# Performance work log

Hardware: AMD Instinct MI355X
Metric: run time of the kernel (lower is better)

## Reference

```python
import jax, jax.numpy as jnp
import numpy as np

D_MODEL, D_K, D_V = 1024, 64, 64
B, S = 4, 4096

def setup_inputs() -> dict:
    key = jax.random.key(0)
    ks = jax.random.split(key, 9)
    s_in = 1.0 / np.sqrt(D_MODEL)
    return {
        "Q": jax.random.normal(ks[0], (B, S, D_MODEL), jnp.float32),
        "K": jax.random.normal(ks[1], (B, S, D_MODEL), jnp.float32),
        "V": jax.random.normal(ks[2], (B, S, D_MODEL), jnp.float32),
        "Wq": jax.random.uniform(ks[3], (D_MODEL, D_K), jnp.float32, -s_in, s_in),
        "bq": jax.random.uniform(ks[4], (D_K,), jnp.float32, -s_in, s_in),
        "Wk": jax.random.uniform(ks[5], (D_MODEL, D_K), jnp.float32, -s_in, s_in),
        "bk": jax.random.uniform(ks[6], (D_K,), jnp.float32, -s_in, s_in),
        "Wv": jax.random.uniform(ks[7], (D_MODEL, D_V), jnp.float32, -s_in, s_in),
        "bv": jax.random.uniform(ks[8], (D_V,), jnp.float32, -s_in, s_in),
    }

def reference(Q, K, V, Wq, bq, Wk, bk, Wv, bv):
    # Linear projections: [B,S,d_model] -> [B,S,d_k/d_v]
    q = jnp.einsum("bsm,mk->bsk", Q, Wq) + bq
    k = jnp.einsum("btm,mk->btk", K, Wk) + bk
    v = jnp.einsum("btm,mv->btv", V, Wv) + bv
    # Scaled dot-product attention, softmax over key axis (dim=2)
    scores = jnp.einsum("bsk,btk->bst", q, k) / jnp.sqrt(jnp.float32(D_K))
    attn = jax.nn.softmax(scores, axis=2)  # [B,S,S]
    return jnp.einsum("bst,btv->bsv", attn, v)
```

## Files before the change

### kernel.cpp

```cpp
#include <hip/hip_runtime.h>

typedef __bf16 bf16;
typedef __attribute__((ext_vector_type(4))) __bf16 bf16x4;
typedef __attribute__((ext_vector_type(8))) __bf16 bf16x8;
typedef __attribute__((ext_vector_type(4))) float f32x4;
typedef __attribute__((ext_vector_type(16))) float f32x16;

#define MFMA16(a, b, c) __builtin_amdgcn_mfma_f32_16x16x32_bf16((a), (b), (c), 0, 0, 0)
#define MFMA32(a, b, c) __builtin_amdgcn_mfma_f32_32x32x16_bf16((a), (b), (c), 0, 0, 0)

__device__ __forceinline__ bf16 tobf(float f) {
    unsigned u = __float_as_uint(f);
    u += 0x7fffu + ((u >> 16) & 1u);
    unsigned short h = (unsigned short)(u >> 16);
    bf16 r;
    __builtin_memcpy(&r, &h, 2);
    return r;
}

__device__ __forceinline__ void stage16(const void* g, void* l) {
    __builtin_amdgcn_global_load_lds(
        (const __attribute__((address_space(1))) unsigned int*)g,
        (__attribute__((address_space(3))) unsigned int*)l, 16, 0, 0);
}

__global__ void wconv_kernel(const float* __restrict__ Wq, const float* __restrict__ Wk,
                             const float* __restrict__ Wv, bf16* __restrict__ Wt) {
    int j = blockIdx.y;
    const float* W = (j == 0) ? Wq : ((j == 1) ? Wk : Wv);
    int idx = blockIdx.x * 256 + threadIdx.x;
    int m = idx >> 6, n = idx & 63;
    Wt[(size_t)j * 65536 + (size_t)n * 1024 + m] = tobf(W[idx]);
}

__launch_bounds__(256, 3)
__global__ void proj_kernel(const float* __restrict__ Q, const float* __restrict__ K,
                            const float* __restrict__ V, const bf16* __restrict__ Wt,
                            const float* __restrict__ bq, const float* __restrict__ bk,
                            const float* __restrict__ bv,
                            bf16* __restrict__ q_ws, bf16* __restrict__ k_ws,
                            bf16* __restrict__ vT_ws) {
    const int j = blockIdx.y;
    const float* In   = (j == 0) ? Q : ((j == 1) ? K : V);
    const float* bias = (j == 0) ? bq : ((j == 1) ? bk : bv);
    const bf16* W = Wt + (size_t)j * 65536;

    __shared__ float As[2][64][64];

    const int tid = threadIdx.x;
    const int wave = tid >> 6, lane = tid & 63;
    const int quad = lane >> 4, l16 = lane & 15;
    const int rbase = blockIdx.x * 64;

    const char* asrc[4];
    char* adst0[4];
    char* adst1[4];
#pragma unroll
    for (int i = 0; i < 4; i++) {
        int u = i * 256 + tid;
        int row = u >> 4;
        int rg = ((u & 15) * 16) ^ ((row & 7) << 4);
        asrc[i] = (const char*)(In + (size_t)(rbase + row) * 1024) + rg;
        adst0[i] = (char*)&As[0][0][0] + u * 16;
        adst1[i] = (char*)&As[1][0][0] + u * 16;
    }

#pragma unroll
    for (int i = 0; i < 4; i++) stage16(asrc[i], adst0[i]);
    __syncthreads();

    f32x4 acc[4];
#pragma unroll
    for (int nt = 0; nt < 4; nt++) acc[nt] = {0.f, 0.f, 0.f, 0.f};

    const int row = wave * 16 + l16;
    const char* arow = (const char*)&As[0][row][0];
    const int sw = (l16 & 7) << 4;
    const bf16* wrow = W + quad * 8;

#pragma unroll 2
    for (int t = 0; t < 16; ++t) {
        const int cur = t & 1;
        if (t < 15) {
#pragma unroll
            for (int i = 0; i < 4; i++)
                stage16(asrc[i] + (t + 1) * 256, cur ? adst0[i] : adst1[i]);
        }
        bf16x8 bf[2][4];
#pragma unroll
        for (int c = 0; c < 2; c++)
#pragma unroll
            for (int nt = 0; nt < 4; nt++)
                bf[c][nt] = *(const bf16x8*)(wrow + (size_t)(nt * 16 + l16) * 1024 +
                                             t * 64 + c * 32);
        const char* ab = arow + (size_t)cur * 16384;
#pragma unroll
        for (int c = 0; c < 2; c++) {
            f32x4 a0 = *(const f32x4*)(ab + ((c * 128 + quad * 32) ^ sw));
            f32x4 a1 = *(const f32x4*)(ab + ((c * 128 + quad * 32 + 16) ^ sw));
            bf16x8 av;
            av[0] = (bf16)a0[0]; av[1] = (bf16)a0[1];
            av[2] = (bf16)a0[2]; av[3] = (bf16)a0[3];
            av[4] = (bf16)a1[0]; av[5] = (bf16)a1[1];
            av[6] = (bf16)a1[2]; av[7] = (bf16)a1[3];
#pragma unroll
            for (int nt = 0; nt < 4; nt++) acc[nt] = MFMA16(av, bf[c][nt], acc[nt]);
        }
        __syncthreads();
    }

    const float scale = (j == 0) ? 0.125f * 1.44269504088896f : 1.0f;

    if (j != 2) {
        bf16* dst = (j == 0) ? q_ws : k_ws;
#pragma unroll
        for (int nt = 0; nt < 4; nt++) {
            int n = nt * 16 + l16;
            float bb = bias[n];
#pragma unroll
            for (int r4 = 0; r4 < 4; r4++) {
                int orow = rbase + wave * 16 + quad * 4 + r4;
                dst[(size_t)orow * 64 + n] = tobf((acc[nt][r4] + bb) * scale);
            }
        }
    } else {
        bf16 (*vtile)[72] = (bf16(*)[72])As;
#pragma unroll
        for (int nt = 0; nt < 4; nt++) {
            int n = nt * 16 + l16;
            float bb = bias[n];
#pragma unroll
            for (int r4 = 0; r4 < 4; r4++) {
                vtile[n][wave * 16 + quad * 4 + r4] = tobf(acc[nt][r4] + bb);
            }
        }
        __syncthreads();
        int bi = rbase >> 12, t0 = rbase & 4095;
        int d = tid >> 2, part = (tid & 3) * 16;
        bf16x8 x0 = *(const bf16x8*)&vtile[d][part];
        bf16x8 x1 = *(const bf16x8*)&vtile[d][part + 8];
        bf16* dst = vT_ws + (size_t)(bi * 64 + d) * 4096 + t0 + part;
        *(bf16x8*)dst = x0;
        *(bf16x8*)(dst + 8) = x1;
    }
}

__launch_bounds__(256, 4)
__global__ void attn_kernel(const bf16* __restrict__ q_ws, const bf16* __restrict__ k_ws,
                            const bf16* __restrict__ vT_ws,
                            float* __restrict__ po, float* __restrict__ pl,
                            float* __restrict__ out, int keys_per_split, int direct) {
    const int b = blockIdx.z, split = blockIdx.y;
    const int tid = threadIdx.x, wave = tid >> 6, lane = tid & 63;
    const int l32 = lane & 31, h = lane >> 5;
    const int sw = l32 & 7;

    __shared__ bf16 kt[64][64];
    __shared__ bf16 vt[64][64];
    __shared__ bf16 pt[4][32][64];

    const int qrow0 = b * 4096 + blockIdx.x * 128 + wave * 32;

    bf16x8 qf[4];
    const bf16* qp = q_ws + (size_t)(qrow0 + l32) * 64 + h * 8;
#pragma unroll
    for (int c = 0; c < 4; c++) qf[c] = *(const bf16x8*)(qp + c * 16);

    f32x16 o0, o1;
    float l_lane = 0.f;
#pragma unroll
    for (int i = 0; i < 16; i++) { o0[i] = 0.f; o1[i] = 0.f; }

    const int key0 = split * keys_per_split;
    const int srow = tid >> 3;
    const int sg = tid & 7;
    const int sgk = sg ^ (srow & 7);
    const bf16* kg = k_ws + (size_t)(b * 4096 + key0 + srow) * 64 + sg * 8;
    const bf16* vg = vT_ws + (size_t)(b * 64 + srow) * 4096 + key0 + sg * 8;

    uint4 kv0 = *(const uint4*)kg;
    uint4 kv1 = *(const uint4*)(kg + 2048);
    uint4 vv0 = *(const uint4*)vg;
    uint4 vv1 = *(const uint4*)(vg + 131072);

    for (int t0 = 0; t0 < keys_per_split; t0 += 64) {
        __syncthreads();
        *(uint4*)&kt[srow][sgk * 8]      = kv0;
        *(uint4*)&kt[srow + 32][sgk * 8] = kv1;
        *(uint4*)&vt[srow][sgk * 8]      = vv0;
        *(uint4*)&vt[srow + 32][sgk * 8] = vv1;
        if (t0 + 64 < keys_per_split) {
            kv0 = *(const uint4*)(kg + (size_t)(t0 + 64) * 64);
            kv1 = *(const uint4*)(kg + (size_t)(t0 + 64) * 64 + 2048);
            vv0 = *(const uint4*)(vg + t0 + 64);
            vv1 = *(const uint4*)(vg + t0 + 64 + 131072);
        }
        __syncthreads();

#pragma unroll
        for (int kt32 = 0; kt32 < 2; kt32++) {
            f32x16 s;
#pragma unroll
            for (int i = 0; i < 16; i++) s[i] = 0.f;
#pragma unroll
            for (int c = 0; c < 4; c++) {
                bf16x8 kf = *(const bf16x8*)(&kt[kt32 * 32 + l32][((2 * c + h) ^ sw) * 8]);
                s = MFMA32(kf, qf[c], s);
            }
#pragma unroll
            for (int g = 0; g < 4; g++) {
                float p0 = __builtin_amdgcn_exp2f(s[4 * g + 0]);
                float p1 = __builtin_amdgcn_exp2f(s[4 * g + 1]);
                float p2 = __builtin_amdgcn_exp2f(s[4 * g + 2]);
                float p3 = __builtin_amdgcn_exp2f(s[4 * g + 3]);
                l_lane += (p0 + p1) + (p2 + p3);
                bf16x4 pk;
                pk[0] = (bf16)p0; pk[1] = (bf16)p1; pk[2] = (bf16)p2; pk[3] = (bf16)p3;
                int gp = (kt32 * 4 + g) ^ sw;
                *(bf16x4*)(&pt[wave][l32][gp * 8 + 4 * h]) = pk;
            }
        }

#pragma unroll
        for (int tc = 0; tc < 4; tc++) {
            int gp = ((2 * tc + h) ^ sw) * 8;
            bf16x8 pf  = *(const bf16x8*)(&pt[wave][l32][gp]);
            bf16x8 vf0 = *(const bf16x8*)(&vt[l32][gp]);
            bf16x8 vf1 = *(const bf16x8*)(&vt[32 + l32][gp]);
            o0 = MFMA32(pf, vf0, o0);
            o1 = MFMA32(pf, vf1, o1);
        }
    }

    l_lane += __shfl_xor(l_lane, 32);

    if (direct) {
        float* orow = out + (size_t)qrow0 * 64;
#pragma unroll
        for (int i = 0; i < 16; i++) {
            int R = (i & 3) + 8 * (i >> 2) + 4 * h;
            float inv = 1.0f / __shfl(l_lane, R);
            orow[(size_t)R * 64 + l32]      = o0[i] * inv;
            orow[(size_t)R * 64 + 32 + l32] = o1[i] * inv;
        }
    } else {
        size_t prow = (size_t)split * 16384 + qrow0;
        float* pob = po + prow * 64;
#pragma unroll
        for (int i = 0; i < 16; i++) {
            int R = (i & 3) + 8 * (i >> 2) + 4 * h;
            pob[(size_t)R * 64 + l32]      = o0[i];
            pob[(size_t)R * 64 + 32 + l32] = o1[i];
        }
        if (h == 0) pl[prow + l32] = l_lane;
    }
}

__launch_bounds__(256)
__global__ void combine_kernel(const float* __restrict__ po, const float* __restrict__ pl,
                               float* __restrict__ out, int nsplit) {
    int idx = blockIdx.x * 256 + threadIdx.x;
    int row = idx >> 6;
    float so = 0.f, sl = 0.f;
    for (int s = 0; s < nsplit; s++) {
        so += po[(size_t)s * 1048576 + idx];
        sl += pl[(size_t)s * 16384 + row];
    }
    out[idx] = so / sl;
}

extern "C" void kernel_launch(void* const* d_in, const int* in_sizes, int n_in,
                              void* d_out, int out_size, void* d_ws, size_t ws_size,
                              hipStream_t stream) {
    const float* Q  = (const float*)d_in[0];
    const float* K  = (const float*)d_in[1];
    const float* V  = (const float*)d_in[2];
    const float* Wq = (const float*)d_in[3];
    const float* bq = (const float*)d_in[4];
    const float* Wk = (const float*)d_in[5];
    const float* bk = (const float*)d_in[6];
    const float* Wv = (const float*)d_in[7];
    const float* bv = (const float*)d_in[8];
    float* out = (float*)d_out;

    char* ws = (char*)d_ws;
    bf16* Wt    = (bf16*)ws;
    bf16* q_ws  = (bf16*)(ws + 393216);
    bf16* k_ws  = (bf16*)(ws + 393216 + 2097152);
    bf16* vT_ws = (bf16*)(ws + 393216 + 2 * 2097152);
    const size_t base = 393216 + 3 * 2097152;

    const size_t per_split = 16384u * 4u + 1048576u * 4u;
    int nsplit = 1;
    if (ws_size >= base + 8 * per_split) nsplit = 8;
    else if (ws_size >= base + 4 * per_split) nsplit = 4;
    else if (ws_size >= base + 2 * per_split) nsplit = 2;

    float* pl = (float*)(ws + base);
    float* po = (float*)(ws + base + (size_t)nsplit * 65536);

    hipLaunchKernelGGL(wconv_kernel, dim3(256, 3), dim3(256), 0, stream, Wq, Wk, Wv, Wt);
    hipLaunchKernelGGL(proj_kernel, dim3(256, 3), dim3(256), 0, stream,
                       Q, K, V, Wt, bq, bk, bv, q_ws, k_ws, vT_ws);
    hipLaunchKernelGGL(attn_kernel, dim3(32, nsplit, 4), dim3(256), 0, stream,
                       q_ws, k_ws, vT_ws, po, pl, out, 4096 / nsplit, nsplit == 1 ? 1 : 0);
    if (nsplit > 1) {
        hipLaunchKernelGGL(combine_kernel, dim3(4096), dim3(256), 0, stream, po, pl, out, nsplit);
    }
}
```

Measured before the change: 254.4 us.

## Replace LDS-staged projection loop with direct-to-register triple-buffered global loads

Drops the LDS double buffer for the projection's fp32 input tiles. Each lane now loads its own A fragments and W fragments straight into registers with inline-asm global_load_dwordx4. A 3-slot register ring is managed with explicit vmcnt waits and sched barriers, so there are no per-iteration __syncthreads. This is meant to remove LDS round-trips and block-wide barriers in a memory-bound projection, at the cost of more VGPRs, less coalesced per-lane access, and fragile hand-managed waitcnt ordering.

```diff
diff --git a/kernel.cpp b/kernel.cpp
--- a/kernel.cpp
+++ b/kernel.cpp
@@ -16,12 +16,6 @@
     bf16 r;
     __builtin_memcpy(&r, &h, 2);
     return r;
-}
-
-__device__ __forceinline__ void stage16(const void* g, void* l) {
-    __builtin_amdgcn_global_load_lds(
-        (const __attribute__((address_space(1))) unsigned int*)g,
-        (__attribute__((address_space(3))) unsigned int*)l, 16, 0, 0);
 }
 
 __global__ void wconv_kernel(const float* __restrict__ Wq, const float* __restrict__ Wk,
@@ -45,69 +39,70 @@
     const float* bias = (j == 0) ? bq : ((j == 1) ? bk : bv);
     const bf16* W = Wt + (size_t)j * 65536;
 
-    __shared__ float As[2][64][64];
+    __shared__ bf16 vtile[64][72];
 
     const int tid = threadIdx.x;
     const int wave = tid >> 6, lane = tid & 63;
     const int quad = lane >> 4, l16 = lane & 15;
     const int rbase = blockIdx.x * 64;
-
-    const char* asrc[4];
-    char* adst0[4];
-    char* adst1[4];
-#pragma unroll
-    for (int i = 0; i < 4; i++) {
-        int u = i * 256 + tid;
-        int row = u >> 4;
-        int rg = ((u & 15) * 16) ^ ((row & 7) << 4);
-        asrc[i] = (const char*)(In + (size_t)(rbase + row) * 1024) + rg;
-        adst0[i] = (char*)&As[0][0][0] + u * 16;
-        adst1[i] = (char*)&As[1][0][0] + u * 16;
-    }
-
-#pragma unroll
-    for (int i = 0; i < 4; i++) stage16(asrc[i], adst0[i]);
-    __syncthreads();
+    const int r0 = rbase + wave * 16;
+
+    unsigned aoff = ((unsigned)(r0 + l16) * 1024u + (unsigned)quad * 8u) * 4u;
+    unsigned boff = ((unsigned)l16 * 1024u + (unsigned)quad * 8u) * 2u;
+    const bf16* Wb0 = W;
+    const bf16* Wb1 = W + 16384;
+    const bf16* Wb2 = W + 32768;
+    const bf16* Wb3 = W + 49152;
+
+    f32x4 a0[3], a1[3];
+    bf16x8 bb[3][4];
+
+#define ISSUE(sl)                                                                          \
+    do {                                                                                   \
+        asm volatile("global_load_dwordx4 %0, %1, %2 offset:0"                             \
+                     : "=v"(a0[sl]) : "v"(aoff), "s"(In));                                 \
+        asm volatile("global_load_dwordx4 %0, %1, %2 offset:16"                            \
+                     : "=v"(a1[sl]) : "v"(aoff), "s"(In));                                 \
+        asm volatile("global_load_dwordx4 %0, %1, %2 offset:0"                             \
+                     : "=v"(bb[sl][0]) : "v"(boff), "s"(Wb0));                             \
+        asm volatile("global_load_dwordx4 %0, %1, %2 offset:0"                             \
+                     : "=v"(bb[sl][1]) : "v"(boff), "s"(Wb1));                             \
+        asm volatile("global_load_dwordx4 %0, %1, %2 offset:0"                             \
+                     : "=v"(bb[sl][2]) : "v"(boff), "s"(Wb2));                             \
+        asm volatile("global_load_dwordx4 %0, %1, %2 offset:0"                             \
+                     : "=v"(bb[sl][3]) : "v"(boff), "s"(Wb3));                             \
+        aoff += 128u;                                                                      \
+        boff += 64u;                                                                       \
+    } while (0)
+
+    ISSUE(0);
+    ISSUE(1);
+    ISSUE(2);
 
     f32x4 acc[4];
 #pragma unroll
     for (int nt = 0; nt < 4; nt++) acc[nt] = {0.f, 0.f, 0.f, 0.f};
 
-    const int row = wave * 16 + l16;
-    const char* arow = (const char*)&As[0][row][0];
-    const int sw = (l16 & 7) << 4;
-    const bf16* wrow = W + quad * 8;
-
-#pragma unroll 2
-    for (int t = 0; t < 16; ++t) {
-        const int cur = t & 1;
-        if (t < 15) {
-#pragma unroll
-            for (int i = 0; i < 4; i++)
-                stage16(asrc[i] + (t + 1) * 256, cur ? adst0[i] : adst1[i]);
-        }
-        bf16x8 bf[2][4];
-#pragma unroll
-        for (int c = 0; c < 2; c++)
-#pragma unroll
-            for (int nt = 0; nt < 4; nt++)
-                bf[c][nt] = *(const bf16x8*)(wrow + (size_t)(nt * 16 + l16) * 1024 +
-                                             t * 64 + c * 32);
-        const char* ab = arow + (size_t)cur * 16384;
-#pragma unroll
-        for (int c = 0; c < 2; c++) {
-            f32x4 a0 = *(const f32x4*)(ab + ((c * 128 + quad * 32) ^ sw));
-            f32x4 a1 = *(const f32x4*)(ab + ((c * 128 + quad * 32 + 16) ^ sw));
-            bf16x8 av;
-            av[0] = (bf16)a0[0]; av[1] = (bf16)a0[1];
-            av[2] = (bf16)a0[2]; av[3] = (bf16)a0[3];
-            av[4] = (bf16)a1[0]; av[5] = (bf16)a1[1];
-            av[6] = (bf16)a1[2]; av[7] = (bf16)a1[3];
-#pragma unroll
-            for (int nt = 0; nt < 4; nt++) acc[nt] = MFMA16(av, bf[c][nt], acc[nt]);
-        }
-        __syncthreads();
-    }
+#pragma unroll
+    for (int s = 0; s < 32; ++s) {
+        const int sl = s % 3;
+        if (s < 30)       asm volatile("s_waitcnt vmcnt(12)" ::: "memory");
+        else if (s == 30) asm volatile("s_waitcnt vmcnt(6)" ::: "memory");
+        else              asm volatile("s_waitcnt vmcnt(0)" ::: "memory");
+        __builtin_amdgcn_sched_barrier(0);
+
+        bf16x8 av;
+        av[0] = (bf16)a0[sl][0]; av[1] = (bf16)a0[sl][1];
+        av[2] = (bf16)a0[sl][2]; av[3] = (bf16)a0[sl][3];
+        av[4] = (bf16)a1[sl][0]; av[5] = (bf16)a1[sl][1];
+        av[6] = (bf16)a1[sl][2]; av[7] = (bf16)a1[sl][3];
+#pragma unroll
+        for (int nt = 0; nt < 4; nt++) acc[nt] = MFMA16(av, bb[sl][nt], acc[nt]);
+
+        __builtin_amdgcn_sched_barrier(0);
+        if (s <= 28) ISSUE(sl);
+    }
+#undef ISSUE
 
     const float scale = (j == 0) ? 0.125f * 1.44269504088896f : 1.0f;
 
@@ -116,22 +111,21 @@
 #pragma unroll
         for (int nt = 0; nt < 4; nt++) {
             int n = nt * 16 + l16;
-            float bb = bias[n];
+            float bb_ = bias[n];
 #pragma unroll
             for (int r4 = 0; r4 < 4; r4++) {
                 int orow = rbase + wave * 16 + quad * 4 + r4;
-                dst[(size_t)orow * 64 + n] = tobf((acc[nt][r4] + bb) * scale);
+                dst[(size_t)orow * 64 + n] = tobf((acc[nt][r4] + bb_) * scale);
             }
         }
     } else {
-        bf16 (*vtile)[72] = (bf16(*)[72])As;
 #pragma unroll
         for (int nt = 0; nt < 4; nt++) {
             int n = nt * 16 + l16;
-            float bb = bias[n];
+            float bb_ = bias[n];
 #pragma unroll
             for (int r4 = 0; r4 < 4; r4++) {
-                vtile[n][wave * 16 + quad * 4 + r4] = tobf(acc[nt][r4] + bb);
+                vtile[n][wave * 16 + quad * 4 + r4] = tobf(acc[nt][r4] + bb_);
             }
         }
         __syncthreads();
```

Measured after the change: 262.4 us. 1.03x slower.

## Restructure projection kernel to stage full 16-row panels with one wave per output column block

Applied to the files above, without the earlier changes.

The projection kernel now gives each block 16 input rows, where it previously took 64. It loads the full 16x1024 fp32 panel into LDS in a single pass and drops the double-buffered K-loop. Each wave computes one 16-column output tile over the full reduction, so the grid grows to 1024x3 blocks. The aim is more blocks in flight to hide HBM latency on a bandwidth-bound fp32 read, at the cost of 64KB LDS per block (lower occupancy), no load/compute overlap within a block, and smaller transposed V stores.

```diff
diff --git a/kernel.cpp b/kernel.cpp
--- a/kernel.cpp
+++ b/kernel.cpp
@@ -33,7 +33,7 @@
     Wt[(size_t)j * 65536 + (size_t)n * 1024 + m] = tobf(W[idx]);
 }
 
-__launch_bounds__(256, 3)
+__launch_bounds__(256, 2)
 __global__ void proj_kernel(const float* __restrict__ Q, const float* __restrict__ K,
                             const float* __restrict__ V, const bf16* __restrict__ Wt,
                             const float* __restrict__ bq, const float* __restrict__ bk,
@@ -45,103 +45,68 @@
     const float* bias = (j == 0) ? bq : ((j == 1) ? bk : bv);
     const bf16* W = Wt + (size_t)j * 65536;
 
-    __shared__ float As[2][64][64];
+    __shared__ float As[16][1024];
 
     const int tid = threadIdx.x;
     const int wave = tid >> 6, lane = tid & 63;
     const int quad = lane >> 4, l16 = lane & 15;
-    const int rbase = blockIdx.x * 64;
-
-    const char* asrc[4];
-    char* adst0[4];
-    char* adst1[4];
-#pragma unroll
-    for (int i = 0; i < 4; i++) {
-        int u = i * 256 + tid;
-        int row = u >> 4;
-        int rg = ((u & 15) * 16) ^ ((row & 7) << 4);
-        asrc[i] = (const char*)(In + (size_t)(rbase + row) * 1024) + rg;
-        adst0[i] = (char*)&As[0][0][0] + u * 16;
-        adst1[i] = (char*)&As[1][0][0] + u * 16;
-    }
-
-#pragma unroll
-    for (int i = 0; i < 4; i++) stage16(asrc[i], adst0[i]);
+    const int r0 = blockIdx.x * 16;
+
+    {
+        const char* pansrc = (const char*)(In + (size_t)r0 * 1024);
+        char* lds0 = (char*)&As[0][0];
+#pragma unroll
+        for (int i = 0; i < 16; i++) {
+            int u = i * 256 + tid;
+            int row = u >> 8, gw = u & 255;
+            int srcoff = row * 4096 + ((gw * 16) ^ ((row & 7) << 4));
+            stage16(pansrc + srcoff, lds0 + u * 16);
+        }
+    }
     __syncthreads();
 
-    f32x4 acc[4];
-#pragma unroll
-    for (int nt = 0; nt < 4; nt++) acc[nt] = {0.f, 0.f, 0.f, 0.f};
-
-    const int row = wave * 16 + l16;
-    const char* arow = (const char*)&As[0][row][0];
+    const char* asb = (const char*)&As[0][0] + l16 * 4096;
     const int sw = (l16 & 7) << 4;
-    const bf16* wrow = W + quad * 8;
-
-#pragma unroll 2
-    for (int t = 0; t < 16; ++t) {
-        const int cur = t & 1;
-        if (t < 15) {
-#pragma unroll
-            for (int i = 0; i < 4; i++)
-                stage16(asrc[i] + (t + 1) * 256, cur ? adst0[i] : adst1[i]);
-        }
-        bf16x8 bf[2][4];
-#pragma unroll
-        for (int c = 0; c < 2; c++)
-#pragma unroll
-            for (int nt = 0; nt < 4; nt++)
-                bf[c][nt] = *(const bf16x8*)(wrow + (size_t)(nt * 16 + l16) * 1024 +
-                                             t * 64 + c * 32);
-        const char* ab = arow + (size_t)cur * 16384;
-#pragma unroll
-        for (int c = 0; c < 2; c++) {
-            f32x4 a0 = *(const f32x4*)(ab + ((c * 128 + quad * 32) ^ sw));
-            f32x4 a1 = *(const f32x4*)(ab + ((c * 128 + quad * 32 + 16) ^ sw));
-            bf16x8 av;
-            av[0] = (bf16)a0[0]; av[1] = (bf16)a0[1];
-            av[2] = (bf16)a0[2]; av[3] = (bf16)a0[3];
-            av[4] = (bf16)a1[0]; av[5] = (bf16)a1[1];
-            av[6] = (bf16)a1[2]; av[7] = (bf16)a1[3];
-#pragma unroll
-            for (int nt = 0; nt < 4; nt++) acc[nt] = MFMA16(av, bf[c][nt], acc[nt]);
-        }
-        __syncthreads();
+    const bf16* wp = W + (size_t)(wave * 16 + l16) * 1024 + quad * 8;
+
+    f32x4 acc = {0.f, 0.f, 0.f, 0.f};
+#pragma unroll
+    for (int s = 0; s < 32; s++) {
+        f32x4 a0 = *(const f32x4*)(asb + s * 128 + ((quad * 32) ^ sw));
+        f32x4 a1 = *(const f32x4*)(asb + s * 128 + ((quad * 32 + 16) ^ sw));
+        bf16x8 bv = *(const bf16x8*)(wp + s * 32);
+        bf16x8 av;
+        av[0] = (bf16)a0[0]; av[1] = (bf16)a0[1];
+        av[2] = (bf16)a0[2]; av[3] = (bf16)a0[3];
+        av[4] = (bf16)a1[0]; av[5] = (bf16)a1[1];
+        av[6] = (bf16)a1[2]; av[7] = (bf16)a1[3];
+        acc = MFMA16(av, bv, acc);
     }
 
     const float scale = (j == 0) ? 0.125f * 1.44269504088896f : 1.0f;
+    const int n = wave * 16 + l16;
+    const float bb = bias[n];
 
     if (j != 2) {
         bf16* dst = (j == 0) ? q_ws : k_ws;
 #pragma unroll
-        for (int nt = 0; nt < 4; nt++) {
-            int n = nt * 16 + l16;
-            float bb = bias[n];
-#pragma unroll
-            for (int r4 = 0; r4 < 4; r4++) {
-                int orow = rbase + wave * 16 + quad * 4 + r4;
-                dst[(size_t)orow * 64 + n] = tobf((acc[nt][r4] + bb) * scale);
-            }
+        for (int r4 = 0; r4 < 4; r4++) {
+            int orow = r0 + quad * 4 + r4;
+            dst[(size_t)orow * 64 + n] = tobf((acc[r4] + bb) * scale);
         }
     } else {
-        bf16 (*vtile)[72] = (bf16(*)[72])As;
-#pragma unroll
-        for (int nt = 0; nt < 4; nt++) {
-            int n = nt * 16 + l16;
-            float bb = bias[n];
-#pragma unroll
-            for (int r4 = 0; r4 < 4; r4++) {
-                vtile[n][wave * 16 + quad * 4 + r4] = tobf(acc[nt][r4] + bb);
-            }
-        }
-        __syncthreads();
-        int bi = rbase >> 12, t0 = rbase & 4095;
-        int d = tid >> 2, part = (tid & 3) * 16;
-        bf16x8 x0 = *(const bf16x8*)&vtile[d][part];
-        bf16x8 x1 = *(const bf16x8*)&vtile[d][part + 8];
+        __syncthreads();
+        bf16 (*vtile)[24] = (bf16(*)[24])As;
+#pragma unroll
+        for (int r4 = 0; r4 < 4; r4++) {
+            vtile[n][quad * 4 + r4] = tobf(acc[r4] + bb);
+        }
+        __syncthreads();
+        int bi = r0 >> 12, t0 = r0 & 4095;
+        int d = tid >> 2, part = (tid & 3) * 4;
+        bf16x4 x = *(const bf16x4*)&vtile[d][part];
         bf16* dst = vT_ws + (size_t)(bi * 64 + d) * 4096 + t0 + part;
-        *(bf16x8*)dst = x0;
-        *(bf16x8*)(dst + 8) = x1;
+        *(bf16x4*)dst = x;
     }
 }
 
@@ -300,7 +265,7 @@
     float* po = (float*)(ws + base + (size_t)nsplit * 65536);
 
     hipLaunchKernelGGL(wconv_kernel, dim3(256, 3), dim3(256), 0, stream, Wq, Wk, Wv, Wt);
-    hipLaunchKernelGGL(proj_kernel, dim3(256, 3), dim3(256), 0, stream,
+    hipLaunchKernelGGL(proj_kernel, dim3(1024, 3), dim3(256), 0, stream,
                        Q, K, V, Wt, bq, bk, bv, q_ws, k_ws, vT_ws);
     hipLaunchKernelGGL(attn_kernel, dim3(32, nsplit, 4), dim3(256), 0, stream,
                        q_ws, k_ws, vT_ws, po, pl, out, 4096 / nsplit, nsplit == 1 ? 1 : 0);
```

Result: no change. 255.1 us (+0.3%).

## Software-pipeline projection GEMM with explicit vmcnt waits and split barriers

Applied to the files above, without the earlier changes.

Restructures the input-projection loop into a fully unrolled double-buffered pipeline with a peeled final tile. The next A tile's async global-to-LDS copy and the W fragment loads are issued before compute. Hand-placed s_waitcnt vmcnt counts and raw s_barrier calls replace the blanket __syncthreads, so W loads stay in flight while waiting only for the current tile. This relies on precise counting of outstanding memory operations, and any miscount could cause races.

```diff
diff --git a/kernel.cpp b/kernel.cpp
--- a/kernel.cpp
+++ b/kernel.cpp
@@ -61,53 +61,77 @@
         int row = u >> 4;
         int rg = ((u & 15) * 16) ^ ((row & 7) << 4);
         asrc[i] = (const char*)(In + (size_t)(rbase + row) * 1024) + rg;
-        adst0[i] = (char*)&As[0][0][0] + u * 16;
-        adst1[i] = (char*)&As[1][0][0] + u * 16;
-    }
+        adst0[i] = (char*)As + u * 16;
+        adst1[i] = (char*)As + 16384 + u * 16;
+    }
+
+    const bf16* wbase = W + (size_t)l16 * 1024 + quad * 8;
 
 #pragma unroll
     for (int i = 0; i < 4; i++) stage16(asrc[i], adst0[i]);
-    __syncthreads();
 
     f32x4 acc[4];
 #pragma unroll
     for (int nt = 0; nt < 4; nt++) acc[nt] = {0.f, 0.f, 0.f, 0.f};
 
-    const int row = wave * 16 + l16;
-    const char* arow = (const char*)&As[0][row][0];
     const int sw = (l16 & 7) << 4;
-    const bf16* wrow = W + quad * 8;
-
-#pragma unroll 2
-    for (int t = 0; t < 16; ++t) {
-        const int cur = t & 1;
-        if (t < 15) {
-#pragma unroll
-            for (int i = 0; i < 4; i++)
-                stage16(asrc[i] + (t + 1) * 256, cur ? adst0[i] : adst1[i]);
-        }
-        bf16x8 bf[2][4];
+    const char* arow = (const char*)As + (size_t)(wave * 16 + l16) * 256;
+
+#define COMPUTE_TILE(AB, BFR)                                                     \
+    do {                                                                          \
+        _Pragma("unroll")                                                         \
+        for (int c = 0; c < 2; c++) {                                             \
+            f32x4 a0 = *(const f32x4*)((AB) + ((c * 128 + quad * 32) ^ sw));      \
+            f32x4 a1 = *(const f32x4*)((AB) + ((c * 128 + quad * 32 + 16) ^ sw)); \
+            bf16x8 av;                                                            \
+            av[0] = (bf16)a0[0]; av[1] = (bf16)a0[1];                             \
+            av[2] = (bf16)a0[2]; av[3] = (bf16)a0[3];                             \
+            av[4] = (bf16)a1[0]; av[5] = (bf16)a1[1];                             \
+            av[6] = (bf16)a1[2]; av[7] = (bf16)a1[3];                             \
+            _Pragma("unroll")                                                     \
+            for (int nt = 0; nt < 4; nt++)                                        \
+                acc[nt] = MFMA16(av, (BFR)[c][nt], acc[nt]);                      \
+        }                                                                         \
+    } while (0)
+
+#pragma unroll
+    for (int t = 0; t < 15; ++t) {
+#pragma unroll
+        for (int i = 0; i < 4; i++)
+            stage16(asrc[i] + (t + 1) * 256, ((t + 1) & 1) ? adst1[i] : adst0[i]);
+        bf16x8 bfr[2][4];
 #pragma unroll
         for (int c = 0; c < 2; c++)
 #pragma unroll
             for (int nt = 0; nt < 4; nt++)
-                bf[c][nt] = *(const bf16x8*)(wrow + (size_t)(nt * 16 + l16) * 1024 +
-                                             t * 64 + c * 32);
-        const char* ab = arow + (size_t)cur * 16384;
-#pragma unroll
-        for (int c = 0; c < 2; c++) {
-            f32x4 a0 = *(const f32x4*)(ab + ((c * 128 + quad * 32) ^ sw));
-            f32x4 a1 = *(const f32x4*)(ab + ((c * 128 + quad * 32 + 16) ^ sw));
-            bf16x8 av;
-            av[0] = (bf16)a0[0]; av[1] = (bf16)a0[1];
-            av[2] = (bf16)a0[2]; av[3] = (bf16)a0[3];
-            av[4] = (bf16)a1[0]; av[5] = (bf16)a1[1];
-            av[6] = (bf16)a1[2]; av[7] = (bf16)a1[3];
-#pragma unroll
-            for (int nt = 0; nt < 4; nt++) acc[nt] = MFMA16(av, bf[c][nt], acc[nt]);
-        }
-        __syncthreads();
-    }
+                bfr[c][nt] = *(const bf16x8*)(wbase + (size_t)nt * 16384 + t * 64 + c * 32);
+
+        asm volatile("s_waitcnt vmcnt(12)" ::: "memory");
+        __builtin_amdgcn_sched_barrier(0);
+        __builtin_amdgcn_s_barrier();
+        asm volatile("s_waitcnt vmcnt(4)" ::: "memory");
+        __builtin_amdgcn_sched_barrier(0);
+
+        COMPUTE_TILE(arow + (t & 1) * 16384, bfr);
+
+        __builtin_amdgcn_s_barrier();
+    }
+
+    {
+        bf16x8 bfr[2][4];
+#pragma unroll
+        for (int c = 0; c < 2; c++)
+#pragma unroll
+            for (int nt = 0; nt < 4; nt++)
+                bfr[c][nt] = *(const bf16x8*)(wbase + (size_t)nt * 16384 + 15 * 64 + c * 32);
+        asm volatile("s_waitcnt vmcnt(8)" ::: "memory");
+        __builtin_amdgcn_sched_barrier(0);
+        __builtin_amdgcn_s_barrier();
+        asm volatile("s_waitcnt vmcnt(0)" ::: "memory");
+        __builtin_amdgcn_sched_barrier(0);
+        COMPUTE_TILE(arow + 16384, bfr);
+    }
+#undef COMPUTE_TILE
 
     const float scale = (j == 0) ? 0.125f * 1.44269504088896f : 1.0f;
 
```

Result: slower. 261.3 us (+2.7%).
